# Kernel optimization log

Measured on AMD Instinct MI355X. Metric: run time of the kernel, lower is better.

Reference implementation:

```python
import jax, jax.numpy as jnp
import numpy as np

B, N, D, DL, DK, DC = 4, 2048, 1024, 64, 128, 8
G_S, G_2, G_1 = 1.0, 0.5, 0.3
EPS = 1e-6

def _christoffel(dk, dl):
    # Poincare-inspired init: for k < min(dk,dl): row/col k set to 0.01, then -0.01 on the diagonal
    G = np.zeros((dk, dl, dl), np.float32)
    idx = np.arange(dl)
    for k in range(min(dk, dl)):
        G[k, k, :] = 0.01
        G[k, :, k] = 0.01
        G[k, idx, idx] -= 0.01
    return jnp.asarray(G)

def setup_inputs() -> dict:
    key = jax.random.key(0)
    ks = jax.random.split(key, 12)
    inp = {
        'x_query': jax.random.normal(ks[0], (B, D), jnp.float32),
        'z_query': 0.1 * jax.random.normal(ks[1], (B, DL), jnp.float32),
        'x_keys': jax.random.normal(ks[2], (B, N, D), jnp.float32),
        'z_keys': 0.1 * jax.random.normal(ks[3], (B, N, DL), jnp.float32),
        'W_Q': jax.random.normal(ks[4], (DK, D), jnp.float32) / np.sqrt(D),
        'W_Qz': jax.random.normal(ks[5], (DK, DL), jnp.float32) / np.sqrt(DL),
        'W_Qgamma': _christoffel(DK, DL),
        'W_K': jax.random.normal(ks[6], (DK, D), jnp.float32) / np.sqrt(D),
        'W_V': jax.random.normal(ks[7], (DK, D), jnp.float32) / np.sqrt(D),
        'W_O': jax.random.normal(ks[8], (D, DK), jnp.float32) / np.sqrt(DK),
        'W_delta': jax.random.normal(ks[9], (DC, DL), jnp.float32) / np.sqrt(DL),
        'basis_b': 0.01 * jax.random.normal(ks[10], (DC, DK, DK), jnp.float32),
        'basis_e': 0.01 * jax.random.normal(ks[11], (DC, DK, DK), jnp.float32),
        'basis_o': 0.01 * jax.random.normal(jax.random.fold_in(key, 99), (DC, DK, DK), jnp.float32),
        'log_sigma': jnp.asarray(np.log(G_S ** 2), jnp.float32),
    }
    return inp

def reference(x_query, z_query, x_keys, z_keys, W_Q, W_Qz, W_Qgamma,
              W_K, W_V, W_O, W_delta, basis_b, basis_e, basis_o, log_sigma):
    dk = W_Q.shape[0]
    # Christoffel query: linear + position + quadratic form  [B, dk]
    q = x_query @ W_Q.T + z_query @ W_Qz.T \
        + jnp.einsum('aij,bi,bj->ba', W_Qgamma, z_query, z_query)
    k = x_keys @ W_K.T            # [B, N, dk]
    v = x_keys @ W_V.T            # [B, N, dk]
    # Wilson line approx: U = I + sum_r coeff_r * (g * skew(basis_r))
    delta = z_query[:, None, :] - z_keys          # [B, N, DL]
    coeff = delta @ W_delta.T                     # [B, N, DC]
    skew = lambda b: b - jnp.swapaxes(b, -1, -2)
    basis = G_S * skew(basis_b) + G_2 * skew(basis_e) + G_1 * skew(basis_o)  # [DC, dk, dk]
    H = jnp.einsum('bnr,rij->bnij', coeff, basis)  # [B, N, dk, dk]
    kt = k + jnp.einsum('bnij,bnj->bni', H, k)     # (I + H) k
    # Conformal temperature tau = sqrt(dk) / lambda(z)
    r_sq = jnp.clip(jnp.sum(z_query ** 2, axis=-1, keepdims=True), None, 1.0 - EPS)
    lam = 2.0 / (1.0 - r_sq + EPS)                 # [B, 1]
    tau = jnp.sqrt(jnp.float32(dk)) / lam
    scores = jnp.einsum('bd,bnd->bn', q, kt) / tau
    attn = jax.nn.softmax(scores, axis=-1)
    # Area-law screening (level=0 -> sigma_eff = sigma)
    dist_sq = jnp.sum(delta ** 2, axis=-1)         # [B, N]
    area = 0.5 * lam ** 2 * dist_sq
    attn = attn * jnp.exp(-jnp.exp(log_sigma) * area)
    out = jnp.einsum('bn,bnd->bd', attn, v) @ W_O.T  # [B, D]
    return out
```

## Files before the change

### kernel.cpp

```cpp
#include <hip/hip_runtime.h>
#include <math.h>


constexpr int AV_OFF   = 0;
constexpr int SC_OFF   = 36864;
constexpr int WZ_OFF   = 36928;
constexpr int DIST_OFF = 102464;
constexpr int S_OFF    = 110656;
constexpr int AEXP_OFF = 118848;
constexpr int W_OFF    = 127040;
constexpr int XBAR_OFF = 135232;
constexpr int QG_OFF   = 139328;
constexpr int QS_OFF   = 139840;
constexpr int US_OFF   = 140352;
constexpr int Y_OFF    = 144448;
constexpr int WS_FLOATS = 144960;

__device__ __forceinline__ float wave_sum(float v) {
#pragma unroll
  for (int off = 32; off > 0; off >>= 1) v += __shfl_xor(v, off, 64);
  return v;
}

__global__ __launch_bounds__(256) void k_init(
    const float* __restrict__ zq_g, const float* __restrict__ z_keys,
    const float* __restrict__ Wd,   const float* __restrict__ G,
    const float* __restrict__ lsig, float* __restrict__ ws) {
  const int tid = threadIdx.x;
  const int blk = blockIdx.x;

  if (blk < 128) {
    __shared__ float szq[256];
    __shared__ float part[1024];
    __shared__ float red2[256];
    szq[tid] = zq_g[tid];
    __syncthreads();
    const int i = tid >> 2, jc = tid & 3;
    const float* Gp = G + blk * 4096 + i * 64 + jc * 16;
    float pb0 = 0, pb1 = 0, pb2 = 0, pb3 = 0;
#pragma unroll
    for (int k = 0; k < 16; ++k) {
      float g = Gp[k];
      int j = jc * 16 + k;
      pb0 += g * szq[0 * 64 + j];
      pb1 += g * szq[1 * 64 + j];
      pb2 += g * szq[2 * 64 + j];
      pb3 += g * szq[3 * 64 + j];
    }
    part[tid * 4 + 0] = pb0; part[tid * 4 + 1] = pb1;
    part[tid * 4 + 2] = pb2; part[tid * 4 + 3] = pb3;
    __syncthreads();
    if (tid < 64) {
#pragma unroll
      for (int b = 0; b < 4; ++b) {
        float s = part[(tid * 4 + 0) * 4 + b] + part[(tid * 4 + 1) * 4 + b] +
                  part[(tid * 4 + 2) * 4 + b] + part[(tid * 4 + 3) * 4 + b];
        red2[tid * 4 + b] = s * szq[b * 64 + tid];
      }
    }
    __syncthreads();
    if (tid < 4) {
      float s = 0;
      for (int i2 = 0; i2 < 64; ++i2) s += red2[i2 * 4 + tid];
      ws[QG_OFF + tid * 128 + blk] = s;
    }
  } else if (blk < 160) {
    __shared__ float sWd[512];
    __shared__ float szq[256];
    sWd[tid] = Wd[tid];
    sWd[256 + tid] = Wd[256 + tid];
    szq[tid] = zq_g[tid];
    __syncthreads();
    const int bn = (blk - 128) * 256 + tid;
    const int b = bn >> 11;
    const float* zk = z_keys + (size_t)bn * 64;
    const float* zq = szq + b * 64;
    float wz[8] = {0, 0, 0, 0, 0, 0, 0, 0};
    float dist = 0;
    for (int l = 0; l < 64; ++l) {
      float z = zk[l];
      float dz = zq[l] - z;
      dist += dz * dz;
#pragma unroll
      for (int r = 0; r < 8; ++r) wz[r] += sWd[r * 64 + l] * z;
    }
#pragma unroll
    for (int r = 0; r < 8; ++r) ws[WZ_OFF + bn * 8 + r] = wz[r];
    ws[DIST_OFF + bn] = dist;
  } else if (blk == 160) {
    __shared__ float szq[256];
    szq[tid] = zq_g[tid];
    __syncthreads();
    const int b = tid >> 6, l = tid & 63;
    float z = szq[b * 64 + l];
    float r2 = wave_sum(z * z);
    float cz[8];
#pragma unroll
    for (int r = 0; r < 8; ++r) cz[r] = wave_sum(Wd[r * 64 + l] * z);
    if (l == 0) {
      r2 = fminf(r2, 1.0f - 1e-6f);
      float lam = 2.0f / (1.0f - r2 + 1e-6f);
      ws[SC_OFF + b * 16 + 0] = lam / sqrtf(128.0f);
      ws[SC_OFF + b * 16 + 1] = expf(lsig[0]) * 0.5f * lam * lam;
#pragma unroll
      for (int r = 0; r < 8; ++r) ws[SC_OFF + b * 16 + 2 + r] = cz[r];
    }
  } else {
    const int b = blk - 161;
    for (int i = tid; i < 1024; i += 256) ws[XBAR_OFF + b * 1024 + i] = 0.0f;
  }
}

__global__ __launch_bounds__(256) void k_q(
    const float* __restrict__ xq_g, const float* __restrict__ zq_g,
    const float* __restrict__ WQ,   const float* __restrict__ WQz,
    float* __restrict__ ws) {
  const int b = blockIdx.x, as_ = blockIdx.y, tid = threadIdx.x;
  __shared__ __align__(16) float xqs[1024];
  __shared__ float zq[64];
  __shared__ float part[256];
  for (int i = tid; i < 1024; i += 256) xqs[i] = xq_g[b * 1024 + i];
  if (tid < 64) zq[tid] = zq_g[b * 64 + tid];
  __syncthreads();

  const int a_loc = tid >> 4, seg = tid & 15;
  const int a = as_ * 16 + a_loc;
  const float4* wq4 = (const float4*)(WQ + a * 1024 + seg * 64);
  const float4* xs4 = (const float4*)(xqs + seg * 64);
  float p = 0;
#pragma unroll
  for (int c = 0; c < 16; ++c) {
    float4 w = wq4[c], x = xs4[c];
    p += w.x * x.x + w.y * x.y + w.z * x.z + w.w * x.w;
  }
#pragma unroll
  for (int c = 0; c < 4; ++c)
    p += WQz[a * 64 + seg * 4 + c] * zq[seg * 4 + c];
  part[tid] = p;
  __syncthreads();
  if (tid < 16) {
    float s = 0;
#pragma unroll
    for (int h = 0; h < 16; ++h) s += part[tid * 16 + h];
    const int aa = as_ * 16 + tid;
    ws[QS_OFF + b * 128 + aa] = s + ws[QG_OFF + b * 128 + aa];
  }
}

__global__ __launch_bounds__(256) void k_u(
    const float* __restrict__ bb, const float* __restrict__ be,
    const float* __restrict__ bo, float* __restrict__ ws) {
  const int r = blockIdx.x, tid = threadIdx.x;
  __shared__ float tmp[128 * 129];
  __shared__ float sq[512];
  __shared__ float red[1024];
  for (int o = tid; o < 512; o += 256) sq[o] = ws[QS_OFF + o];
  __syncthreads();

  const int j = tid & 127, half = tid >> 7;
  float acc[4] = {0, 0, 0, 0};
  const float* arrs[3] = {bb, be, bo};
  const float wgt[3] = {1.0f, 0.5f, 0.3f};

  for (int arr = 0; arr < 3; ++arr) {
    const float4* src = (const float4*)(arrs[arr] + r * 16384);
    for (int idx = tid; idx < 4096; idx += 256) {
      float4 v = src[idx];
      const int i = idx >> 5, col = (idx & 31) * 4;
      float* dst = tmp + i * 129 + col;
      dst[0] = v.x; dst[1] = v.y; dst[2] = v.z; dst[3] = v.w;
    }
    __syncthreads();
    const float w = wgt[arr];
    for (int ii = 0; ii < 64; ++ii) {
      const int i = half * 64 + ii;
      const float d = w * (tmp[i * 129 + j] - tmp[j * 129 + i]);
#pragma unroll
      for (int b = 0; b < 4; ++b) acc[b] += d * sq[b * 128 + i];
    }
    __syncthreads();
  }
#pragma unroll
  for (int b = 0; b < 4; ++b) red[half * 512 + b * 128 + j] = acc[b];
  __syncthreads();
  for (int o = tid; o < 512; o += 256) {
    const int b = o >> 7, jj = o & 127;
    ws[US_OFF + b * 1024 + r * 128 + jj] = red[o] + red[512 + o];
  }
}

__global__ __launch_bounds__(256) void k_av(
    const float* __restrict__ WK, float* __restrict__ ws) {
  const int b = blockIdx.x, dbase = blockIdx.y * 64, tid = threadIdx.x;
  __shared__ float qu[1152];
  __shared__ float part[2304];
  __shared__ float fin[576];
  __shared__ float czq[8];
  for (int o = tid; o < 1152; o += 256)
    qu[o] = (o < 128) ? ws[QS_OFF + b * 128 + o]
                      : ws[US_OFF + b * 1024 + (o - 128)];
  if (tid < 8) czq[tid] = ws[SC_OFF + b * 16 + 2 + tid];
  __syncthreads();

  const int kq = tid >> 6, dloc = tid & 63;
  float acc[9];
#pragma unroll
  for (int jj = 0; jj < 9; ++jj) acc[jj] = 0;
  const float* wkp = WK + dbase + dloc;
#pragma unroll 4
  for (int k = kq * 32; k < kq * 32 + 32; ++k) {
    const float wk = wkp[k * 1024];
#pragma unroll
    for (int jj = 0; jj < 9; ++jj) acc[jj] += qu[jj * 128 + k] * wk;
  }
#pragma unroll
  for (int jj = 0; jj < 9; ++jj) part[kq * 576 + jj * 64 + dloc] = acc[jj];
  __syncthreads();
  for (int o = tid; o < 576; o += 256)
    fin[o] = part[o] + part[576 + o] + part[1152 + o] + part[1728 + o];
  __syncthreads();
  float* av = ws + AV_OFF + b * 9216;
  for (int o = tid; o < 576; o += 256) {
    const int jj = o >> 6, dl = o & 63;
    float val = fin[o];
    if (jj == 0) {
#pragma unroll
      for (int rr = 0; rr < 8; ++rr) val += czq[rr] * fin[(1 + rr) * 64 + dl];
    }
    av[jj * 1024 + dbase + dl] = val;
  }
}

__global__ __launch_bounds__(256) void k2_scores(
    const float* __restrict__ x_keys, float* __restrict__ ws) {
  __shared__ __align__(16) float sav[9216];
  __shared__ float s_sc[2];
  const int tid = threadIdx.x;
  const int b = blockIdx.y;
  const float* avg = ws + AV_OFF + b * 9216;
  for (int i = tid * 4; i < 9216; i += 1024)
    *(float4*)(sav + i) = *(const float4*)(avg + i);
  if (tid < 2) s_sc[tid] = ws[SC_OFF + b * 16 + tid];
  __syncthreads();

  const int wave = tid >> 6, lane = tid & 63;
  const int nbase = blockIdx.x * 16 + wave * 4;
  const float* xb = x_keys + ((size_t)(b * 2048 + nbase)) * 1024;

  float acc[9][4];
#pragma unroll
  for (int j = 0; j < 9; ++j)
#pragma unroll
    for (int p = 0; p < 4; ++p) acc[j][p] = 0;

#pragma unroll
  for (int c = 0; c < 4; ++c) {
    const int off = c * 256 + lane * 4;
    float4 xv[4];
#pragma unroll
    for (int p = 0; p < 4; ++p)
      xv[p] = *(const float4*)(xb + p * 1024 + off);
#pragma unroll
    for (int j = 0; j < 9; ++j) {
      float4 a = *(const float4*)(sav + j * 1024 + off);
#pragma unroll
      for (int p = 0; p < 4; ++p)
        acc[j][p] += a.x * xv[p].x + a.y * xv[p].y + a.z * xv[p].z + a.w * xv[p].w;
    }
  }
#pragma unroll
  for (int j = 0; j < 9; ++j)
#pragma unroll
    for (int p = 0; p < 4; ++p) acc[j][p] = wave_sum(acc[j][p]);

  if (lane == 0) {
    const float it = s_sc[0], sc = s_sc[1];
    for (int p = 0; p < 4; ++p) {
      const int bn = b * 2048 + nbase + p;
      const float* wz = ws + WZ_OFF + bn * 8;
      float s = acc[0][p];
#pragma unroll
      for (int r = 0; r < 8; ++r) s -= wz[r] * acc[1 + r][p];
      ws[S_OFF + bn] = s * it;
      ws[AEXP_OFF + bn] = sc * ws[DIST_OFF + bn];
    }
  }
}

__global__ __launch_bounds__(256) void k3_softmax(float* __restrict__ ws) {
  const int b = blockIdx.x, tid = threadIdx.x;
  __shared__ float red[256];
  float sv[8];
  float vmax = -1e30f;
#pragma unroll
  for (int i = 0; i < 8; ++i) {
    sv[i] = ws[S_OFF + b * 2048 + i * 256 + tid];
    vmax = fmaxf(vmax, sv[i]);
  }
  red[tid] = vmax;
  __syncthreads();
  for (int s = 128; s > 0; s >>= 1) {
    if (tid < s) red[tid] = fmaxf(red[tid], red[tid + s]);
    __syncthreads();
  }
  const float m = red[0];
  __syncthreads();
  float lsum = 0;
#pragma unroll
  for (int i = 0; i < 8; ++i) lsum += expf(sv[i] - m);
  red[tid] = lsum;
  __syncthreads();
  for (int s = 128; s > 0; s >>= 1) {
    if (tid < s) red[tid] += red[tid + s];
    __syncthreads();
  }
  const float rl = 1.0f / red[0];
#pragma unroll
  for (int i = 0; i < 8; ++i) {
    const int idx = b * 2048 + i * 256 + tid;
    ws[W_OFF + idx] = expf(sv[i] - m - ws[AEXP_OFF + idx]) * rl;
  }
}

__global__ __launch_bounds__(256) void k4_xbar(
    const float* __restrict__ x_keys, float* __restrict__ ws) {
  const int tid = threadIdx.x;
  const int nt = blockIdx.x, dsl = blockIdx.y, b = blockIdx.z;
  __shared__ float sw[256];
  const int n0 = nt * 256;
  sw[tid] = ws[W_OFF + b * 2048 + n0 + tid];
  __syncthreads();
  const int d = dsl * 256 + tid;
  const float* xb = x_keys + ((size_t)(b * 2048 + n0)) * 1024 + d;
  float a0 = 0, a1 = 0, a2 = 0, a3 = 0;
  for (int n = 0; n < 256; n += 4) {
    a0 += sw[n + 0] * xb[(size_t)(n + 0) * 1024];
    a1 += sw[n + 1] * xb[(size_t)(n + 1) * 1024];
    a2 += sw[n + 2] * xb[(size_t)(n + 2) * 1024];
    a3 += sw[n + 3] * xb[(size_t)(n + 3) * 1024];
  }
  atomicAdd(&ws[XBAR_OFF + b * 1024 + d], (a0 + a1) + (a2 + a3));
}

__global__ __launch_bounds__(256) void k5a_y(
    const float* __restrict__ WV, float* __restrict__ ws) {
  const int b = blockIdx.x, sl = blockIdx.y, tid = threadIdx.x;
  __shared__ __align__(16) float sx[1024];
  __shared__ float part[256];
  for (int i = tid; i < 1024; i += 256) sx[i] = ws[XBAR_OFF + b * 1024 + i];
  __syncthreads();
  const int dk_loc = tid >> 4, seg = tid & 15;
  const int dk = sl * 16 + dk_loc;
  const float4* wv4 = (const float4*)(WV + dk * 1024 + seg * 64);
  const float4* xs4 = (const float4*)(sx + seg * 64);
  float p = 0;
#pragma unroll
  for (int c = 0; c < 16; ++c) {
    float4 w = wv4[c], x = xs4[c];
    p += w.x * x.x + w.y * x.y + w.z * x.z + w.w * x.w;
  }
  part[tid] = p;
  __syncthreads();
  if (tid < 16) {
    float s = 0;
#pragma unroll
    for (int h = 0; h < 16; ++h) s += part[tid * 16 + h];
    ws[Y_OFF + b * 128 + sl * 16 + tid] = s;
  }
}

__global__ __launch_bounds__(256) void k5b_out(
    const float* __restrict__ WO, const float* __restrict__ ws,
    float* __restrict__ out) {
  const int b = blockIdx.x, dsl = blockIdx.y, tid = threadIdx.x;
  __shared__ float sy[128];
  if (tid < 128) sy[tid] = ws[Y_OFF + b * 128 + tid];
  __syncthreads();
  const int d = dsl * 256 + tid;
  const float4* wo4 = (const float4*)(WO + d * 128);
  float acc = 0;
#pragma unroll
  for (int c = 0; c < 32; ++c) {
    float4 w = wo4[c];
    acc += w.x * sy[c * 4 + 0] + w.y * sy[c * 4 + 1] +
           w.z * sy[c * 4 + 2] + w.w * sy[c * 4 + 3];
  }
  out[b * 1024 + d] = acc;
}

extern "C" void kernel_launch(void* const* d_in, const int* in_sizes, int n_in,
                              void* d_out, int out_size, void* d_ws,
                              size_t ws_size, hipStream_t stream) {
  const float* xq  = (const float*)d_in[0];
  const float* zq  = (const float*)d_in[1];
  const float* xk  = (const float*)d_in[2];
  const float* zk  = (const float*)d_in[3];
  const float* WQ  = (const float*)d_in[4];
  const float* WQz = (const float*)d_in[5];
  const float* G   = (const float*)d_in[6];
  const float* WK  = (const float*)d_in[7];
  const float* WV  = (const float*)d_in[8];
  const float* WO  = (const float*)d_in[9];
  const float* Wd  = (const float*)d_in[10];
  const float* bb  = (const float*)d_in[11];
  const float* be  = (const float*)d_in[12];
  const float* bo  = (const float*)d_in[13];
  const float* ls  = (const float*)d_in[14];
  float* ws  = (float*)d_ws;
  float* out = (float*)d_out;
  if (ws_size < (size_t)WS_FLOATS * sizeof(float)) return;

  hipLaunchKernelGGL(k_init, dim3(165), dim3(256), 0, stream,
                     zq, zk, Wd, G, ls, ws);
  hipLaunchKernelGGL(k_q, dim3(4, 8), dim3(256), 0, stream,
                     xq, zq, WQ, WQz, ws);
  hipLaunchKernelGGL(k_u, dim3(8), dim3(256), 0, stream, bb, be, bo, ws);
  hipLaunchKernelGGL(k_av, dim3(4, 16), dim3(256), 0, stream, WK, ws);
  hipLaunchKernelGGL(k2_scores, dim3(128, 4), dim3(256), 0, stream, xk, ws);
  hipLaunchKernelGGL(k3_softmax, dim3(4), dim3(256), 0, stream, ws);
  hipLaunchKernelGGL(k4_xbar, dim3(8, 4, 4), dim3(256), 0, stream, xk, ws);
  hipLaunchKernelGGL(k5a_y, dim3(4, 8), dim3(256), 0, stream, WV, ws);
  hipLaunchKernelGGL(k5b_out, dim3(4, 4), dim3(256), 0, stream, WO, ws, out);
}
```

Measured before the change: 168.0 us.

## Fuse all stages into one persistent kernel with grid-wide barriers

Replaces nine separate kernel launches with a single 256-block kernel. Stages are separated by atomic-counter grid barriers, and a memset zeroes the accumulator and barrier counters. It also redistributes work: the Christoffel quadratic term is folded into the q computation, the U projection is spread over 64 blocks, and the softmax is fused with the weighted x_keys reduction. This removes launch gaps and the intermediate round trips, at the cost of spin-wait barriers that rely on all 256 blocks being resident at once and on blocks redundantly recomputing the softmax statistics.

```diff
diff --git a/kernel.cpp b/kernel.cpp
--- a/kernel.cpp
+++ b/kernel.cpp
@@ -2,19 +2,18 @@
 #include <math.h>
 
 
-constexpr int AV_OFF   = 0;
-constexpr int SC_OFF   = 36864;
-constexpr int WZ_OFF   = 36928;
-constexpr int DIST_OFF = 102464;
-constexpr int S_OFF    = 110656;
-constexpr int AEXP_OFF = 118848;
-constexpr int W_OFF    = 127040;
-constexpr int XBAR_OFF = 135232;
-constexpr int QG_OFF   = 139328;
-constexpr int QS_OFF   = 139840;
-constexpr int US_OFF   = 140352;
-constexpr int Y_OFF    = 144448;
-constexpr int WS_FLOATS = 144960;
+constexpr int XBAR_OFF = 0;
+constexpr int BAR_OFF  = 4096;
+constexpr int SC_OFF   = 4112;
+constexpr int QS_OFF   = 4176;
+constexpr int US_OFF   = 4688;
+constexpr int AV_OFF   = 8784;
+constexpr int WZ_OFF   = 45648;
+constexpr int DIST_OFF = 111184;
+constexpr int S_OFF    = 119376;
+constexpr int WS_FLOATS = 127568;
+
+constexpr int NBLK = 256;
 
 __device__ __forceinline__ float wave_sum(float v) {
 #pragma unroll
@@ -22,77 +21,109 @@
   return v;
 }
 
-__global__ __launch_bounds__(256) void k_init(
-    const float* __restrict__ zq_g, const float* __restrict__ z_keys,
-    const float* __restrict__ Wd,   const float* __restrict__ G,
-    const float* __restrict__ lsig, float* __restrict__ ws) {
+__device__ __forceinline__ void gsync(int* bar, int phase) {
+  __syncthreads();
+  if (threadIdx.x == 0) {
+    __threadfence();
+    atomicAdd(bar + phase, 1);
+    while (atomicAdd(bar + phase, 0) < NBLK) __builtin_amdgcn_s_sleep(8);
+    __threadfence();
+  }
+  __syncthreads();
+}
+
+__global__ __launch_bounds__(256) void k_fused(
+    const float* __restrict__ xq, const float* __restrict__ zq,
+    const float* __restrict__ x_keys, const float* __restrict__ z_keys,
+    const float* __restrict__ WQ, const float* __restrict__ WQz,
+    const float* __restrict__ G, const float* __restrict__ WK,
+    const float* __restrict__ WV, const float* __restrict__ WO,
+    const float* __restrict__ Wd, const float* __restrict__ bb,
+    const float* __restrict__ be, const float* __restrict__ bo,
+    const float* __restrict__ lsig, float* __restrict__ ws,
+    float* __restrict__ out) {
+  __shared__ __align__(16) float shm[9824];
   const int tid = threadIdx.x;
   const int blk = blockIdx.x;
-
-  if (blk < 128) {
-    __shared__ float szq[256];
-    __shared__ float part[1024];
-    __shared__ float red2[256];
-    szq[tid] = zq_g[tid];
-    __syncthreads();
-    const int i = tid >> 2, jc = tid & 3;
-    const float* Gp = G + blk * 4096 + i * 64 + jc * 16;
-    float pb0 = 0, pb1 = 0, pb2 = 0, pb3 = 0;
-#pragma unroll
-    for (int k = 0; k < 16; ++k) {
-      float g = Gp[k];
-      int j = jc * 16 + k;
-      pb0 += g * szq[0 * 64 + j];
-      pb1 += g * szq[1 * 64 + j];
-      pb2 += g * szq[2 * 64 + j];
-      pb3 += g * szq[3 * 64 + j];
-    }
-    part[tid * 4 + 0] = pb0; part[tid * 4 + 1] = pb1;
-    part[tid * 4 + 2] = pb2; part[tid * 4 + 3] = pb3;
-    __syncthreads();
-    if (tid < 64) {
-#pragma unroll
-      for (int b = 0; b < 4; ++b) {
-        float s = part[(tid * 4 + 0) * 4 + b] + part[(tid * 4 + 1) * 4 + b] +
-                  part[(tid * 4 + 2) * 4 + b] + part[(tid * 4 + 3) * 4 + b];
-        red2[tid * 4 + b] = s * szq[b * 64 + tid];
-      }
-    }
-    __syncthreads();
-    if (tid < 4) {
+  int* bar = (int*)(ws + BAR_OFF);
+
+  if (blk < 32) {
+    float* xqs = shm;
+    float* zqs = shm + 1024;
+    float* part = shm + 1088;
+    const int b = blk >> 3, as_ = blk & 7;
+    for (int i = tid; i < 1024; i += 256) xqs[i] = xq[b * 1024 + i];
+    if (tid < 64) zqs[tid] = zq[b * 64 + tid];
+    __syncthreads();
+    const int seg = tid & 15;
+    const int a = as_ * 16 + (tid >> 4);
+    const float4* wq4 = (const float4*)(WQ + a * 1024 + seg * 64);
+    const float4* xs4 = (const float4*)(xqs + seg * 64);
+    float p = 0;
+#pragma unroll
+    for (int c = 0; c < 16; ++c) {
+      float4 w = wq4[c], x = xs4[c];
+      p += w.x * x.x + w.y * x.y + w.z * x.z + w.w * x.w;
+    }
+#pragma unroll
+    for (int c = 0; c < 4; ++c)
+      p += WQz[a * 64 + seg * 4 + c] * zqs[seg * 4 + c];
+#pragma unroll
+    for (int ii = 0; ii < 4; ++ii) {
+      const int i = seg * 4 + ii;
+      const float4* g4 = (const float4*)(G + a * 4096 + i * 64);
+      float inner = 0;
+#pragma unroll
+      for (int c = 0; c < 16; ++c) {
+        float4 gv = g4[c];
+        const float4 zv = *(const float4*)(zqs + c * 4);
+        inner += gv.x * zv.x + gv.y * zv.y + gv.z * zv.z + gv.w * zv.w;
+      }
+      p += zqs[i] * inner;
+    }
+    part[tid] = p;
+    __syncthreads();
+    if (tid < 16) {
       float s = 0;
-      for (int i2 = 0; i2 < 64; ++i2) s += red2[i2 * 4 + tid];
-      ws[QG_OFF + tid * 128 + blk] = s;
-    }
-  } else if (blk < 160) {
-    __shared__ float sWd[512];
-    __shared__ float szq[256];
+#pragma unroll
+      for (int h = 0; h < 16; ++h) s += part[tid * 16 + h];
+      ws[QS_OFF + b * 128 + as_ * 16 + tid] = s;
+    }
+  } else if (blk < 64) {
+    float* sWd = shm;
+    float* zqs = shm + 512;
     sWd[tid] = Wd[tid];
     sWd[256 + tid] = Wd[256 + tid];
-    szq[tid] = zq_g[tid];
-    __syncthreads();
-    const int bn = (blk - 128) * 256 + tid;
+    zqs[tid] = zq[tid];
+    __syncthreads();
+    const int bn = (blk - 32) * 256 + tid;
     const int b = bn >> 11;
-    const float* zk = z_keys + (size_t)bn * 64;
-    const float* zq = szq + b * 64;
-    float wz[8] = {0, 0, 0, 0, 0, 0, 0, 0};
+    const float4* zk4 = (const float4*)(z_keys + (size_t)bn * 64);
+    const float* zqb = zqs + b * 64;
+    float wzv[8] = {0, 0, 0, 0, 0, 0, 0, 0};
     float dist = 0;
-    for (int l = 0; l < 64; ++l) {
-      float z = zk[l];
-      float dz = zq[l] - z;
-      dist += dz * dz;
-#pragma unroll
-      for (int r = 0; r < 8; ++r) wz[r] += sWd[r * 64 + l] * z;
-    }
-#pragma unroll
-    for (int r = 0; r < 8; ++r) ws[WZ_OFF + bn * 8 + r] = wz[r];
+    for (int l4 = 0; l4 < 16; ++l4) {
+      float4 z4 = zk4[l4];
+      float ze[4] = {z4.x, z4.y, z4.z, z4.w};
+#pragma unroll
+      for (int e = 0; e < 4; ++e) {
+        const int l = l4 * 4 + e;
+        float z = ze[e];
+        float dz = zqb[l] - z;
+        dist += dz * dz;
+#pragma unroll
+        for (int r = 0; r < 8; ++r) wzv[r] += sWd[r * 64 + l] * z;
+      }
+    }
+#pragma unroll
+    for (int r = 0; r < 8; ++r) ws[WZ_OFF + bn * 8 + r] = wzv[r];
     ws[DIST_OFF + bn] = dist;
-  } else if (blk == 160) {
-    __shared__ float szq[256];
-    szq[tid] = zq_g[tid];
+  } else if (blk == 64) {
+    float* zqs = shm;
+    zqs[tid] = zq[tid];
     __syncthreads();
     const int b = tid >> 6, l = tid & 63;
-    float z = szq[b * 64 + l];
+    float z = zqs[b * 64 + l];
     float r2 = wave_sum(z * z);
     float cz[8];
 #pragma unroll
@@ -105,287 +136,225 @@
 #pragma unroll
       for (int r = 0; r < 8; ++r) ws[SC_OFF + b * 16 + 2 + r] = cz[r];
     }
-  } else {
-    const int b = blk - 161;
-    for (int i = tid; i < 1024; i += 256) ws[XBAR_OFF + b * 1024 + i] = 0.0f;
-  }
-}
-
-__global__ __launch_bounds__(256) void k_q(
-    const float* __restrict__ xq_g, const float* __restrict__ zq_g,
-    const float* __restrict__ WQ,   const float* __restrict__ WQz,
-    float* __restrict__ ws) {
-  const int b = blockIdx.x, as_ = blockIdx.y, tid = threadIdx.x;
-  __shared__ __align__(16) float xqs[1024];
-  __shared__ float zq[64];
-  __shared__ float part[256];
-  for (int i = tid; i < 1024; i += 256) xqs[i] = xq_g[b * 1024 + i];
-  if (tid < 64) zq[tid] = zq_g[b * 64 + tid];
-  __syncthreads();
-
-  const int a_loc = tid >> 4, seg = tid & 15;
-  const int a = as_ * 16 + a_loc;
-  const float4* wq4 = (const float4*)(WQ + a * 1024 + seg * 64);
-  const float4* xs4 = (const float4*)(xqs + seg * 64);
-  float p = 0;
-#pragma unroll
-  for (int c = 0; c < 16; ++c) {
-    float4 w = wq4[c], x = xs4[c];
-    p += w.x * x.x + w.y * x.y + w.z * x.z + w.w * x.w;
-  }
-#pragma unroll
-  for (int c = 0; c < 4; ++c)
-    p += WQz[a * 64 + seg * 4 + c] * zq[seg * 4 + c];
-  part[tid] = p;
-  __syncthreads();
-  if (tid < 16) {
-    float s = 0;
-#pragma unroll
-    for (int h = 0; h < 16; ++h) s += part[tid * 16 + h];
-    const int aa = as_ * 16 + tid;
-    ws[QS_OFF + b * 128 + aa] = s + ws[QG_OFF + b * 128 + aa];
-  }
-}
-
-__global__ __launch_bounds__(256) void k_u(
-    const float* __restrict__ bb, const float* __restrict__ be,
-    const float* __restrict__ bo, float* __restrict__ ws) {
-  const int r = blockIdx.x, tid = threadIdx.x;
-  __shared__ float tmp[128 * 129];
-  __shared__ float sq[512];
-  __shared__ float red[1024];
-  for (int o = tid; o < 512; o += 256) sq[o] = ws[QS_OFF + o];
-  __syncthreads();
-
-  const int j = tid & 127, half = tid >> 7;
-  float acc[4] = {0, 0, 0, 0};
-  const float* arrs[3] = {bb, be, bo};
-  const float wgt[3] = {1.0f, 0.5f, 0.3f};
-
-  for (int arr = 0; arr < 3; ++arr) {
-    const float4* src = (const float4*)(arrs[arr] + r * 16384);
-    for (int idx = tid; idx < 4096; idx += 256) {
-      float4 v = src[idx];
-      const int i = idx >> 5, col = (idx & 31) * 4;
-      float* dst = tmp + i * 129 + col;
-      dst[0] = v.x; dst[1] = v.y; dst[2] = v.z; dst[3] = v.w;
-    }
-    __syncthreads();
-    const float w = wgt[arr];
-    for (int ii = 0; ii < 64; ++ii) {
-      const int i = half * 64 + ii;
-      const float d = w * (tmp[i * 129 + j] - tmp[j * 129 + i]);
-#pragma unroll
-      for (int b = 0; b < 4; ++b) acc[b] += d * sq[b * 128 + i];
-    }
-    __syncthreads();
-  }
-#pragma unroll
-  for (int b = 0; b < 4; ++b) red[half * 512 + b * 128 + j] = acc[b];
-  __syncthreads();
-  for (int o = tid; o < 512; o += 256) {
-    const int b = o >> 7, jj = o & 127;
-    ws[US_OFF + b * 1024 + r * 128 + jj] = red[o] + red[512 + o];
-  }
-}
-
-__global__ __launch_bounds__(256) void k_av(
-    const float* __restrict__ WK, float* __restrict__ ws) {
-  const int b = blockIdx.x, dbase = blockIdx.y * 64, tid = threadIdx.x;
-  __shared__ float qu[1152];
-  __shared__ float part[2304];
-  __shared__ float fin[576];
-  __shared__ float czq[8];
-  for (int o = tid; o < 1152; o += 256)
-    qu[o] = (o < 128) ? ws[QS_OFF + b * 128 + o]
-                      : ws[US_OFF + b * 1024 + (o - 128)];
-  if (tid < 8) czq[tid] = ws[SC_OFF + b * 16 + 2 + tid];
-  __syncthreads();
-
-  const int kq = tid >> 6, dloc = tid & 63;
-  float acc[9];
-#pragma unroll
-  for (int jj = 0; jj < 9; ++jj) acc[jj] = 0;
-  const float* wkp = WK + dbase + dloc;
+  }
+  gsync(bar, 0);
+
+  if (blk < 64) {
+    const int r = blk >> 3, jc = blk & 7;
+    float* sq = shm;
+    float* red = shm + 512;
+    for (int o = tid; o < 512; o += 256) sq[o] = ws[QS_OFF + o];
+    __syncthreads();
+    const int jl = tid & 15, is = tid >> 4;
+    const int j = jc * 16 + jl;
+    float acc[4] = {0, 0, 0, 0};
+    const float* arrs[3] = {bb, be, bo};
+    const float wgt[3] = {1.0f, 0.5f, 0.3f};
+#pragma unroll
+    for (int arr = 0; arr < 3; ++arr) {
+      const float w = wgt[arr];
+      const float* base = arrs[arr] + r * 16384;
+#pragma unroll
+      for (int k = 0; k < 8; ++k) {
+        const int i = is * 8 + k;
+        const float sk = w * (base[i * 128 + j] - base[j * 128 + i]);
+#pragma unroll
+        for (int b = 0; b < 4; ++b) acc[b] += sk * sq[b * 128 + i];
+      }
+    }
+#pragma unroll
+    for (int b = 0; b < 4; ++b) red[(jl * 4 + b) * 16 + is] = acc[b];
+    __syncthreads();
+    if (tid < 64) {
+      const int jl2 = tid >> 2, b = tid & 3;
+      float s = 0;
+#pragma unroll
+      for (int is2 = 0; is2 < 16; ++is2) s += red[(jl2 * 4 + b) * 16 + is2];
+      ws[US_OFF + b * 1024 + r * 128 + jc * 16 + jl2] = s;
+    }
+  }
+  gsync(bar, 1);
+
+  if (blk < 64) {
+    const int b = blk >> 4, dbase = (blk & 15) * 64;
+    float* qu = shm;
+    float* part = shm + 1152;
+    float* fin = shm + 3456;
+    float* czq = shm + 4032;
+    for (int o = tid; o < 1152; o += 256)
+      qu[o] = (o < 128) ? ws[QS_OFF + b * 128 + o]
+                        : ws[US_OFF + b * 1024 + (o - 128)];
+    if (tid < 8) czq[tid] = ws[SC_OFF + b * 16 + 2 + tid];
+    __syncthreads();
+    const int kq = tid >> 6, dloc = tid & 63;
+    float acc[9];
+#pragma unroll
+    for (int jj = 0; jj < 9; ++jj) acc[jj] = 0;
+    const float* wkp = WK + dbase + dloc;
 #pragma unroll 4
-  for (int k = kq * 32; k < kq * 32 + 32; ++k) {
-    const float wk = wkp[k * 1024];
-#pragma unroll
-    for (int jj = 0; jj < 9; ++jj) acc[jj] += qu[jj * 128 + k] * wk;
-  }
-#pragma unroll
-  for (int jj = 0; jj < 9; ++jj) part[kq * 576 + jj * 64 + dloc] = acc[jj];
-  __syncthreads();
-  for (int o = tid; o < 576; o += 256)
-    fin[o] = part[o] + part[576 + o] + part[1152 + o] + part[1728 + o];
-  __syncthreads();
-  float* av = ws + AV_OFF + b * 9216;
-  for (int o = tid; o < 576; o += 256) {
-    const int jj = o >> 6, dl = o & 63;
-    float val = fin[o];
-    if (jj == 0) {
-#pragma unroll
-      for (int rr = 0; rr < 8; ++rr) val += czq[rr] * fin[(1 + rr) * 64 + dl];
-    }
-    av[jj * 1024 + dbase + dl] = val;
-  }
-}
-
-__global__ __launch_bounds__(256) void k2_scores(
-    const float* __restrict__ x_keys, float* __restrict__ ws) {
-  __shared__ __align__(16) float sav[9216];
-  __shared__ float s_sc[2];
-  const int tid = threadIdx.x;
-  const int b = blockIdx.y;
-  const float* avg = ws + AV_OFF + b * 9216;
-  for (int i = tid * 4; i < 9216; i += 1024)
-    *(float4*)(sav + i) = *(const float4*)(avg + i);
-  if (tid < 2) s_sc[tid] = ws[SC_OFF + b * 16 + tid];
-  __syncthreads();
-
-  const int wave = tid >> 6, lane = tid & 63;
-  const int nbase = blockIdx.x * 16 + wave * 4;
-  const float* xb = x_keys + ((size_t)(b * 2048 + nbase)) * 1024;
-
-  float acc[9][4];
-#pragma unroll
-  for (int j = 0; j < 9; ++j)
-#pragma unroll
-    for (int p = 0; p < 4; ++p) acc[j][p] = 0;
-
-#pragma unroll
-  for (int c = 0; c < 4; ++c) {
-    const int off = c * 256 + lane * 4;
-    float4 xv[4];
-#pragma unroll
-    for (int p = 0; p < 4; ++p)
-      xv[p] = *(const float4*)(xb + p * 1024 + off);
-#pragma unroll
-    for (int j = 0; j < 9; ++j) {
-      float4 a = *(const float4*)(sav + j * 1024 + off);
-#pragma unroll
-      for (int p = 0; p < 4; ++p)
-        acc[j][p] += a.x * xv[p].x + a.y * xv[p].y + a.z * xv[p].z + a.w * xv[p].w;
-    }
-  }
-#pragma unroll
-  for (int j = 0; j < 9; ++j)
-#pragma unroll
-    for (int p = 0; p < 4; ++p) acc[j][p] = wave_sum(acc[j][p]);
-
-  if (lane == 0) {
-    const float it = s_sc[0], sc = s_sc[1];
-    for (int p = 0; p < 4; ++p) {
-      const int bn = b * 2048 + nbase + p;
-      const float* wz = ws + WZ_OFF + bn * 8;
-      float s = acc[0][p];
-#pragma unroll
-      for (int r = 0; r < 8; ++r) s -= wz[r] * acc[1 + r][p];
-      ws[S_OFF + bn] = s * it;
-      ws[AEXP_OFF + bn] = sc * ws[DIST_OFF + bn];
-    }
-  }
-}
-
-__global__ __launch_bounds__(256) void k3_softmax(float* __restrict__ ws) {
-  const int b = blockIdx.x, tid = threadIdx.x;
-  __shared__ float red[256];
-  float sv[8];
-  float vmax = -1e30f;
-#pragma unroll
-  for (int i = 0; i < 8; ++i) {
-    sv[i] = ws[S_OFF + b * 2048 + i * 256 + tid];
-    vmax = fmaxf(vmax, sv[i]);
-  }
-  red[tid] = vmax;
-  __syncthreads();
-  for (int s = 128; s > 0; s >>= 1) {
-    if (tid < s) red[tid] = fmaxf(red[tid], red[tid + s]);
-    __syncthreads();
-  }
-  const float m = red[0];
-  __syncthreads();
-  float lsum = 0;
-#pragma unroll
-  for (int i = 0; i < 8; ++i) lsum += expf(sv[i] - m);
-  red[tid] = lsum;
-  __syncthreads();
-  for (int s = 128; s > 0; s >>= 1) {
-    if (tid < s) red[tid] += red[tid + s];
-    __syncthreads();
-  }
-  const float rl = 1.0f / red[0];
-#pragma unroll
-  for (int i = 0; i < 8; ++i) {
-    const int idx = b * 2048 + i * 256 + tid;
-    ws[W_OFF + idx] = expf(sv[i] - m - ws[AEXP_OFF + idx]) * rl;
-  }
-}
-
-__global__ __launch_bounds__(256) void k4_xbar(
-    const float* __restrict__ x_keys, float* __restrict__ ws) {
-  const int tid = threadIdx.x;
-  const int nt = blockIdx.x, dsl = blockIdx.y, b = blockIdx.z;
-  __shared__ float sw[256];
-  const int n0 = nt * 256;
-  sw[tid] = ws[W_OFF + b * 2048 + n0 + tid];
-  __syncthreads();
-  const int d = dsl * 256 + tid;
-  const float* xb = x_keys + ((size_t)(b * 2048 + n0)) * 1024 + d;
-  float a0 = 0, a1 = 0, a2 = 0, a3 = 0;
-  for (int n = 0; n < 256; n += 4) {
-    a0 += sw[n + 0] * xb[(size_t)(n + 0) * 1024];
-    a1 += sw[n + 1] * xb[(size_t)(n + 1) * 1024];
-    a2 += sw[n + 2] * xb[(size_t)(n + 2) * 1024];
-    a3 += sw[n + 3] * xb[(size_t)(n + 3) * 1024];
-  }
-  atomicAdd(&ws[XBAR_OFF + b * 1024 + d], (a0 + a1) + (a2 + a3));
-}
-
-__global__ __launch_bounds__(256) void k5a_y(
-    const float* __restrict__ WV, float* __restrict__ ws) {
-  const int b = blockIdx.x, sl = blockIdx.y, tid = threadIdx.x;
-  __shared__ __align__(16) float sx[1024];
-  __shared__ float part[256];
-  for (int i = tid; i < 1024; i += 256) sx[i] = ws[XBAR_OFF + b * 1024 + i];
-  __syncthreads();
-  const int dk_loc = tid >> 4, seg = tid & 15;
-  const int dk = sl * 16 + dk_loc;
-  const float4* wv4 = (const float4*)(WV + dk * 1024 + seg * 64);
-  const float4* xs4 = (const float4*)(sx + seg * 64);
-  float p = 0;
-#pragma unroll
-  for (int c = 0; c < 16; ++c) {
-    float4 w = wv4[c], x = xs4[c];
-    p += w.x * x.x + w.y * x.y + w.z * x.z + w.w * x.w;
-  }
-  part[tid] = p;
-  __syncthreads();
-  if (tid < 16) {
-    float s = 0;
-#pragma unroll
-    for (int h = 0; h < 16; ++h) s += part[tid * 16 + h];
-    ws[Y_OFF + b * 128 + sl * 16 + tid] = s;
-  }
-}
-
-__global__ __launch_bounds__(256) void k5b_out(
-    const float* __restrict__ WO, const float* __restrict__ ws,
-    float* __restrict__ out) {
-  const int b = blockIdx.x, dsl = blockIdx.y, tid = threadIdx.x;
-  __shared__ float sy[128];
-  if (tid < 128) sy[tid] = ws[Y_OFF + b * 128 + tid];
-  __syncthreads();
-  const int d = dsl * 256 + tid;
-  const float4* wo4 = (const float4*)(WO + d * 128);
-  float acc = 0;
-#pragma unroll
-  for (int c = 0; c < 32; ++c) {
-    float4 w = wo4[c];
-    acc += w.x * sy[c * 4 + 0] + w.y * sy[c * 4 + 1] +
-           w.z * sy[c * 4 + 2] + w.w * sy[c * 4 + 3];
-  }
-  out[b * 1024 + d] = acc;
+    for (int k = kq * 32; k < kq * 32 + 32; ++k) {
+      const float wk = wkp[k * 1024];
+#pragma unroll
+      for (int jj = 0; jj < 9; ++jj) acc[jj] += qu[jj * 128 + k] * wk;
+    }
+#pragma unroll
+    for (int jj = 0; jj < 9; ++jj) part[kq * 576 + jj * 64 + dloc] = acc[jj];
+    __syncthreads();
+    for (int o = tid; o < 576; o += 256)
+      fin[o] = part[o] + part[576 + o] + part[1152 + o] + part[1728 + o];
+    __syncthreads();
+    float* av = ws + AV_OFF + b * 9216;
+    for (int o = tid; o < 576; o += 256) {
+      const int jj = o >> 6, dl = o & 63;
+      float val = fin[o];
+      if (jj == 0) {
+#pragma unroll
+        for (int rr = 0; rr < 8; ++rr)
+          val += czq[rr] * fin[(1 + rr) * 64 + dl];
+      }
+      av[jj * 1024 + dbase + dl] = val;
+    }
+  }
+  gsync(bar, 2);
+
+  {
+    float* sav = shm;
+    const int b = blk >> 6;
+    const float* avg = ws + AV_OFF + b * 9216;
+    for (int i = tid * 4; i < 9216; i += 1024)
+      *(float4*)(sav + i) = *(const float4*)(avg + i);
+    if (tid == 0) shm[9216] = ws[SC_OFF + b * 16];
+    __syncthreads();
+
+    const int wave = tid >> 6, lane = tid & 63;
+    for (int half = 0; half < 2; ++half) {
+      const int nbase = (blk & 63) * 32 + half * 16 + wave * 4;
+      const float* xb = x_keys + ((size_t)(b * 2048 + nbase)) * 1024;
+
+      float acc[9][4];
+#pragma unroll
+      for (int j = 0; j < 9; ++j)
+#pragma unroll
+        for (int p = 0; p < 4; ++p) acc[j][p] = 0;
+
+#pragma unroll
+      for (int c = 0; c < 4; ++c) {
+        const int off = c * 256 + lane * 4;
+        float4 xv[4];
+#pragma unroll
+        for (int p = 0; p < 4; ++p)
+          xv[p] = *(const float4*)(xb + p * 1024 + off);
+#pragma unroll
+        for (int j = 0; j < 9; ++j) {
+          float4 a = *(const float4*)(sav + j * 1024 + off);
+#pragma unroll
+          for (int p = 0; p < 4; ++p)
+            acc[j][p] +=
+                a.x * xv[p].x + a.y * xv[p].y + a.z * xv[p].z + a.w * xv[p].w;
+        }
+      }
+#pragma unroll
+      for (int j = 0; j < 9; ++j)
+#pragma unroll
+        for (int p = 0; p < 4; ++p) acc[j][p] = wave_sum(acc[j][p]);
+
+      if (lane == 0) {
+        const float it = shm[9216];
+        for (int p = 0; p < 4; ++p) {
+          const int bn = b * 2048 + nbase + p;
+          const float* wz = ws + WZ_OFF + bn * 8;
+          float s = acc[0][p];
+#pragma unroll
+          for (int r = 0; r < 8; ++r) s -= wz[r] * acc[1 + r][p];
+          ws[S_OFF + bn] = s * it;
+        }
+      }
+    }
+  }
+  gsync(bar, 3);
+
+  {
+    const int b = blk >> 6, loc = blk & 63, nt = loc >> 2, dsl = loc & 3;
+    float* red = shm;
+    float* sw = shm + 256;
+    float sv[8];
+    float vmax = -1e30f;
+#pragma unroll
+    for (int i = 0; i < 8; ++i) {
+      sv[i] = ws[S_OFF + b * 2048 + i * 256 + tid];
+      vmax = fmaxf(vmax, sv[i]);
+    }
+    red[tid] = vmax;
+    __syncthreads();
+    for (int s = 128; s > 0; s >>= 1) {
+      if (tid < s) red[tid] = fmaxf(red[tid], red[tid + s]);
+      __syncthreads();
+    }
+    const float m = red[0];
+    __syncthreads();
+    float lsum = 0;
+#pragma unroll
+    for (int i = 0; i < 8; ++i) lsum += expf(sv[i] - m);
+    red[tid] = lsum;
+    __syncthreads();
+    for (int s = 128; s > 0; s >>= 1) {
+      if (tid < s) red[tid] += red[tid + s];
+      __syncthreads();
+    }
+    const float rl = 1.0f / red[0];
+    const float screen = ws[SC_OFF + b * 16 + 1];
+    const int n0 = nt * 128;
+    if (tid < 128) {
+      const int n = n0 + tid;
+      sw[tid] = expf(ws[S_OFF + b * 2048 + n] - m -
+                     screen * ws[DIST_OFF + b * 2048 + n]) * rl;
+    }
+    __syncthreads();
+    const int d = dsl * 256 + tid;
+    const float* xb = x_keys + ((size_t)(b * 2048 + n0)) * 1024 + d;
+    float a0 = 0, a1 = 0, a2 = 0, a3 = 0;
+    for (int n = 0; n < 128; n += 4) {
+      a0 += sw[n + 0] * xb[(size_t)(n + 0) * 1024];
+      a1 += sw[n + 1] * xb[(size_t)(n + 1) * 1024];
+      a2 += sw[n + 2] * xb[(size_t)(n + 2) * 1024];
+      a3 += sw[n + 3] * xb[(size_t)(n + 3) * 1024];
+    }
+    atomicAdd(&ws[XBAR_OFF + b * 1024 + d], (a0 + a1) + (a2 + a3));
+  }
+  gsync(bar, 4);
+
+  if (blk < 16) {
+    const int b = blk >> 2, dsl = blk & 3;
+    float* sx = shm;
+    float* sy = shm + 1024;
+    for (int i = tid; i < 1024; i += 256) sx[i] = ws[XBAR_OFF + b * 1024 + i];
+    __syncthreads();
+    const int wave = tid >> 6, lane = tid & 63;
+    for (int t = 0; t < 32; ++t) {
+      const int dk = wave * 32 + t;
+      const float4* wv4 = (const float4*)(WV + dk * 1024 + lane * 16);
+      const float4* xs4 = (const float4*)(sx + lane * 16);
+      float p = 0;
+#pragma unroll
+      for (int c = 0; c < 4; ++c) {
+        float4 w4 = wv4[c], x4 = xs4[c];
+        p += w4.x * x4.x + w4.y * x4.y + w4.z * x4.z + w4.w * x4.w;
+      }
+      p = wave_sum(p);
+      if (lane == 0) sy[dk] = p;
+    }
+    __syncthreads();
+    const int d = dsl * 256 + tid;
+    const float4* wo4 = (const float4*)(WO + d * 128);
+    float acc = 0;
+#pragma unroll
+    for (int c = 0; c < 32; ++c) {
+      float4 w = wo4[c];
+      acc += w.x * sy[c * 4 + 0] + w.y * sy[c * 4 + 1] +
+             w.z * sy[c * 4 + 2] + w.w * sy[c * 4 + 3];
+    }
+    out[b * 1024 + d] = acc;
+  }
 }
 
 extern "C" void kernel_launch(void* const* d_in, const int* in_sizes, int n_in,
@@ -410,15 +379,9 @@
   float* out = (float*)d_out;
   if (ws_size < (size_t)WS_FLOATS * sizeof(float)) return;
 
-  hipLaunchKernelGGL(k_init, dim3(165), dim3(256), 0, stream,
-                     zq, zk, Wd, G, ls, ws);
-  hipLaunchKernelGGL(k_q, dim3(4, 8), dim3(256), 0, stream,
-                     xq, zq, WQ, WQz, ws);
-  hipLaunchKernelGGL(k_u, dim3(8), dim3(256), 0, stream, bb, be, bo, ws);
-  hipLaunchKernelGGL(k_av, dim3(4, 16), dim3(256), 0, stream, WK, ws);
-  hipLaunchKernelGGL(k2_scores, dim3(128, 4), dim3(256), 0, stream, xk, ws);
-  hipLaunchKernelGGL(k3_softmax, dim3(4), dim3(256), 0, stream, ws);
-  hipLaunchKernelGGL(k4_xbar, dim3(8, 4, 4), dim3(256), 0, stream, xk, ws);
-  hipLaunchKernelGGL(k5a_y, dim3(4, 8), dim3(256), 0, stream, WV, ws);
-  hipLaunchKernelGGL(k5b_out, dim3(4, 4), dim3(256), 0, stream, WO, ws, out);
+  hipMemsetAsync(ws, 0, (size_t)(4096 + 16) * sizeof(float), stream);
+
+  hipLaunchKernelGGL(k_fused, dim3(NBLK), dim3(256), 0, stream,
+                     xq, zq, xk, zk, WQ, WQz, G, WK, WV, WO, Wd, bb, be, bo,
+                     ls, ws, out);
 }
```

Result: slower. 245.7 us (+46.3%).
